# Kernel tuning notes

Measured on AMD Instinct MI355X. Metric: run time of the kernel, lower is better.

The kernel has to match this reference:

```python
import jax, jax.numpy as jnp
import numpy as np

N_NODES = 100000
N_EDGES = 3200000
D_FEAT = 128
N_CLASSES = 40


def setup_inputs() -> dict:
    key = jax.random.key(0)
    k1, k2, k3, k4 = jax.random.split(key, 4)
    x = jax.random.normal(k1, (N_NODES, D_FEAT), dtype=jnp.float32)
    edge_index = jax.random.randint(k2, (2, N_EDGES), 0, N_NODES, dtype=jnp.int64)
    # torch.nn.Linear default init ~ U(-1/sqrt(fan_in), 1/sqrt(fan_in)); randn is fine for a numeric baseline
    W = jax.random.normal(k3, (N_CLASSES, D_FEAT), dtype=jnp.float32) * (1.0 / np.sqrt(D_FEAT))
    b = jax.random.normal(k4, (N_CLASSES,), dtype=jnp.float32) * 0.01
    return {"x": x, "edge_index": edge_index, "W": W, "b": b, "K": 2}


def _sgc_forward(x, edge_index, W, b, K):
    N = x.shape[0]
    loop = jnp.arange(N, dtype=edge_index.dtype)
    # Outer add_self_loops in SGC.forward, then gcn_norm inside SGConv adds
    # self-loops AGAIN (PyG default add_self_loops=True) -> two self-loops per node.
    row = jnp.concatenate([edge_index[0], loop, loop])
    col = jnp.concatenate([edge_index[1], loop, loop])
    # gcn_norm: deg over destination (col) with unit edge weights
    deg = jax.ops.segment_sum(jnp.ones_like(row, dtype=x.dtype), col, num_segments=N)
    dinv = jnp.where(deg > 0, deg ** -0.5, 0.0)
    norm = dinv[row] * dinv[col]  # [E+2N]
    for _ in range(K):
        # out[col] += norm * x[row]  (K-hop symmetric-normalized propagation)
        x = jax.ops.segment_sum(norm[:, None] * x[row], col, num_segments=N)
    logits = x @ W.T + b  # [N, C]
    return jax.nn.log_softmax(logits, axis=1)


def reference(x, edge_index, W, b, K):
    return _sgc_forward(x, edge_index, W, b, K)
```

## Files before the change

### kernel.cpp

```cpp
#include <hip/hip_runtime.h>
#include <hip/hip_bf16.h>
#include <math.h>

#define DF 128
#define NC 40
#define PC 20
#define RB 8
#define RSZ 256
#define CHUNK 4096
#define CAP 12288

typedef float f32x4 __attribute__((ext_vector_type(4)));

__device__ __forceinline__ float bf2f(unsigned short h) {
  unsigned int u = ((unsigned int)h) << 16;
  union { unsigned int u; float f; } c; c.u = u; return c.f;
}
__device__ __forceinline__ unsigned short f2bf(float x) {
  union { float f; unsigned int u; } c; c.f = x;
  unsigned int u = c.u;
  return (unsigned short)((u + 0x7fffu + ((u >> 16) & 1u)) >> 16);
}
__device__ __forceinline__ float blo(unsigned int u) {
  union { unsigned int u; float f; } c; c.u = u << 16; return c.f;
}
__device__ __forceinline__ float bhi(unsigned int u) {
  union { unsigned int u; float f; } c; c.u = u & 0xffff0000u; return c.f;
}

__global__ __launch_bounds__(512) void k_binB(
    const int* __restrict__ row, const int* __restrict__ col,
    int* __restrict__ cnt, unsigned int* __restrict__ slab, int E, int NB) {
  __shared__ int colS[CHUNK];
  __shared__ int hist[512];
  __shared__ int cursor[512];
  int t = threadIdx.x;
  if (t < NB) hist[t] = 0;
  int s = blockIdx.x * CHUNK, e = min(E, s + CHUNK), n = e - s;
  for (int i = t; i < n; i += 512) colS[i] = col[s + i];
  __syncthreads();
  for (int i = t; i < n; i += 512) atomicAdd(&hist[colS[i] >> RB], 1);
  __syncthreads();
  if (t < NB) cursor[t] = hist[t] ? atomicAdd(&cnt[t], hist[t]) : 0;
  __syncthreads();
  for (int i = t; i < n; i += 512) {
    int c = colS[i];
    int b = c >> RB;
    int p = atomicAdd(&cursor[b], 1);
    slab[(size_t)b * CAP + p] = ((unsigned int)row[s + i] << RB) | (unsigned int)(c & (RSZ - 1));
  }
}

__global__ __launch_bounds__(512) void k_bucket_scan(
    const int* __restrict__ cnt, int* __restrict__ base,
    int* __restrict__ off, int NB, int N, int E) {
  __shared__ int s[512];
  int t = threadIdx.x;
  int v = (t < NB) ? cnt[t] : 0;
  s[t] = v;
  __syncthreads();
  for (int o = 1; o < 512; o <<= 1) {
    int u = (t >= o) ? s[t - o] : 0;
    __syncthreads();
    s[t] += u;
    __syncthreads();
  }
  if (t < NB) base[t] = s[t] - v;
  if (t == 0) { base[NB] = E; off[N] = E; }
}

__global__ __launch_bounds__(512) void k_binC(
    const unsigned int* __restrict__ slab, const int* __restrict__ base,
    int* __restrict__ off, int* __restrict__ eidx, float* __restrict__ dinv, int N) {
  __shared__ int hist[RSZ];
  __shared__ int sc[RSZ];
  __shared__ int cur[RSZ];
  int b = blockIdx.x;
  int t = threadIdx.x;
  if (t < RSZ) hist[t] = 0;
  __syncthreads();
  int cb = base[b], ce = base[b + 1];
  int cnt_b = ce - cb;
  const unsigned int* src = slab + (size_t)b * CAP;
  for (int i = t; i < cnt_b; i += 512) atomicAdd(&hist[src[i] & (RSZ - 1)], 1);
  __syncthreads();
  int v = (t < RSZ) ? hist[t] : 0;
  if (t < RSZ) sc[t] = v;
  __syncthreads();
  for (int o = 1; o < RSZ; o <<= 1) {
    int u = (t < RSZ && t >= o) ? sc[t - o] : 0;
    __syncthreads();
    if (t < RSZ) sc[t] += u;
    __syncthreads();
  }
  if (t < RSZ) {
    int pos = cb + sc[t] - v;
    int node = (b << RB) + t;
    if (node < N) {
      off[node] = pos;
      dinv[node] = rsqrtf((float)v + 2.0f);
    }
    cur[t] = pos;
  }
  __syncthreads();
  for (int i = t; i < cnt_b; i += 512) {
    unsigned int en = src[i];
    int p = atomicAdd(&cur[en & (RSZ - 1)], 1);
    eidx[p] = (int)(en >> RB);
  }
}

__global__ __launch_bounds__(128) void k_xw_scale(
    const float* __restrict__ x, const float* __restrict__ W,
    const float* __restrict__ dinv, unsigned short* __restrict__ g0, int N) {
  __shared__ float4 Ws[NC * (DF / 4)];
  for (int i = threadIdx.x; i < NC * (DF / 4); i += blockDim.x)
    Ws[i] = ((const float4*)W)[i];
  __syncthreads();
  int node = blockIdx.x * blockDim.x + threadIdx.x;
  if (node >= N) return;
  float acc[NC];
#pragma unroll
  for (int c = 0; c < NC; ++c) acc[c] = 0.f;
  const float4* xr = (const float4*)(x + (size_t)node * DF);
#pragma unroll 1
  for (int ch = 0; ch < 8; ++ch) {
    float4 v0 = xr[ch * 4 + 0];
    float4 v1 = xr[ch * 4 + 1];
    float4 v2 = xr[ch * 4 + 2];
    float4 v3 = xr[ch * 4 + 3];
#pragma unroll
    for (int c = 0; c < NC; ++c) {
      float4 w0 = Ws[c * (DF / 4) + ch * 4 + 0];
      float4 w1 = Ws[c * (DF / 4) + ch * 4 + 1];
      float4 w2 = Ws[c * (DF / 4) + ch * 4 + 2];
      float4 w3 = Ws[c * (DF / 4) + ch * 4 + 3];
      acc[c] += (v0.x * w0.x + v0.y * w0.y + v0.z * w0.z + v0.w * w0.w) +
                (v1.x * w1.x + v1.y * w1.y + v1.z * w1.z + v1.w * w1.w) +
                (v2.x * w2.x + v2.y * w2.y + v2.z * w2.z + v2.w * w2.w) +
                (v3.x * w3.x + v3.y * w3.y + v3.z * w3.z + v3.w * w3.w);
    }
  }
  float di = dinv[node];
  unsigned int pk[NC / 2];
#pragma unroll
  for (int c2 = 0; c2 < NC / 2; ++c2) {
    unsigned int lo = f2bf(di * acc[c2 * 2 + 0]);
    unsigned int hi = f2bf(di * acc[c2 * 2 + 1]);
    pk[c2] = lo | (hi << 16);
  }
  uint2* p0 = (uint2*)g0 + (size_t)node * 5;
  uint2* p1 = (uint2*)g0 + (size_t)N * 5 + (size_t)node * 5;
#pragma unroll
  for (int q = 0; q < 5; ++q) {
    p0[q] = make_uint2(pk[2 * q], pk[2 * q + 1]);
    p1[q] = make_uint2(pk[10 + 2 * q], pk[10 + 2 * q + 1]);
  }
}

template<int FINAL>
__global__ __launch_bounds__(256) void k_hop(
    const int* __restrict__ off, const int* __restrict__ eidx,
    const float* __restrict__ dinv, const unsigned short* __restrict__ gin,
    unsigned short* __restrict__ gout, float* __restrict__ logits,
    const float* __restrict__ bias, int N, int NBH) {
  int bid = blockIdx.x;
  int slot8 = bid & 7;
  int half = slot8 >> 2;
  int nbi = ((bid >> 3) << 2) + (slot8 & 3);
  if (nbi >= NBH) return;
  int lane = threadIdx.x & 63;
  int nA = (nbi << 3) + ((threadIdx.x >> 6) << 1);
  if (nA >= N) return;
  bool hasB = (nA + 1) < N;
  int nBs = hasB ? nA + 1 : nA;
  int slot = lane / 5;
  unsigned j = (unsigned)(lane - slot * 5);
  bool act = slot < 12;
  const uint2* plane = (const uint2*)gin + (size_t)half * ((size_t)N * 5);
  int sA = __builtin_amdgcn_readfirstlane(off[nA]);
  int eA = __builtin_amdgcn_readfirstlane(off[nA + 1]);
  int sB = eA;
  int eB = eA;
  if (hasB) eB = __builtin_amdgcn_readfirstlane(off[nA + 2]);
  float diA = dinv[nA];
  float diB = dinv[nBs];
  float4 bb;
  if (FINAL) bb = ((const float4*)bias)[half * 5 + (int)j];
  float A0 = 0.f, A1 = 0.f, A2 = 0.f, A3 = 0.f, A4 = 0.f, A5 = 0.f, A6 = 0.f, A7 = 0.f;
  float B0 = 0.f, B1 = 0.f, B2 = 0.f, B3 = 0.f, B4 = 0.f, B5 = 0.f, B6 = 0.f, B7 = 0.f;
  unsigned selfA = (unsigned)nA * 5u + j;
  unsigned selfB = (unsigned)nBs * 5u + j;
  if (slot == 0) {
    uint2 vA = plane[selfA];
    uint2 vB = plane[selfB];
    A0 = 2.f * blo(vA.x); A1 = 2.f * bhi(vA.x); A2 = 2.f * blo(vA.y); A3 = 2.f * bhi(vA.y);
    B0 = 2.f * blo(vB.x); B1 = 2.f * bhi(vB.x); B2 = 2.f * blo(vB.y); B3 = 2.f * bhi(vB.y);
  }
  int lastA = (eA > sA) ? eA - 1 : 0;
  int lastB = (eB > sB) ? eB - 1 : 0;
  {
    int pa0 = sA + slot, pa1 = pa0 + 12, pa2 = pa0 + 24, pa3 = pa0 + 36;
    int pb0 = sB + slot, pb1 = pb0 + 12, pb2 = pb0 + 24, pb3 = pb0 + 36;
    int ra0 = __builtin_nontemporal_load(eidx + min(pa0, lastA));
    int ra1 = __builtin_nontemporal_load(eidx + min(pa1, lastA));
    int ra2 = __builtin_nontemporal_load(eidx + min(pa2, lastA));
    int ra3 = __builtin_nontemporal_load(eidx + min(pa3, lastA));
    int rb0 = __builtin_nontemporal_load(eidx + min(pb0, lastB));
    int rb1 = __builtin_nontemporal_load(eidx + min(pb1, lastB));
    int rb2 = __builtin_nontemporal_load(eidx + min(pb2, lastB));
    int rb3 = __builtin_nontemporal_load(eidx + min(pb3, lastB));
    uint2 va0 = plane[(unsigned)ra0 * 5u + j];
    uint2 va1 = plane[(unsigned)ra1 * 5u + j];
    uint2 va2 = plane[(unsigned)ra2 * 5u + j];
    uint2 va3 = plane[(unsigned)ra3 * 5u + j];
    uint2 vb0 = plane[(unsigned)rb0 * 5u + j];
    uint2 vb1 = plane[(unsigned)rb1 * 5u + j];
    uint2 vb2 = plane[(unsigned)rb2 * 5u + j];
    uint2 vb3 = plane[(unsigned)rb3 * 5u + j];
    float ma0 = (act && pa0 < eA) ? 1.f : 0.f;
    float ma1 = (act && pa1 < eA) ? 1.f : 0.f;
    float ma2 = (act && pa2 < eA) ? 1.f : 0.f;
    float ma3 = (act && pa3 < eA) ? 1.f : 0.f;
    float mb0 = (act && pb0 < eB) ? 1.f : 0.f;
    float mb1 = (act && pb1 < eB) ? 1.f : 0.f;
    float mb2 = (act && pb2 < eB) ? 1.f : 0.f;
    float mb3 = (act && pb3 < eB) ? 1.f : 0.f;
    A0 += ma0 * blo(va0.x); A1 += ma0 * bhi(va0.x); A2 += ma0 * blo(va0.y); A3 += ma0 * bhi(va0.y);
    A0 += ma1 * blo(va1.x); A1 += ma1 * bhi(va1.x); A2 += ma1 * blo(va1.y); A3 += ma1 * bhi(va1.y);
    A4 += ma2 * blo(va2.x); A5 += ma2 * bhi(va2.x); A6 += ma2 * blo(va2.y); A7 += ma2 * bhi(va2.y);
    A4 += ma3 * blo(va3.x); A5 += ma3 * bhi(va3.x); A6 += ma3 * blo(va3.y); A7 += ma3 * bhi(va3.y);
    B0 += mb0 * blo(vb0.x); B1 += mb0 * bhi(vb0.x); B2 += mb0 * blo(vb0.y); B3 += mb0 * bhi(vb0.y);
    B0 += mb1 * blo(vb1.x); B1 += mb1 * bhi(vb1.x); B2 += mb1 * blo(vb1.y); B3 += mb1 * bhi(vb1.y);
    B4 += mb2 * blo(vb2.x); B5 += mb2 * bhi(vb2.x); B6 += mb2 * blo(vb2.y); B7 += mb2 * bhi(vb2.y);
    B4 += mb3 * blo(vb3.x); B5 += mb3 * bhi(vb3.x); B6 += mb3 * blo(vb3.y); B7 += mb3 * bhi(vb3.y);
  }
  for (int i = sA + 48; i < eA; i += 12) {
    int p = i + slot;
    int r = __builtin_nontemporal_load(eidx + min(p, lastA));
    uint2 v = plane[(unsigned)r * 5u + j];
    float m = (act && p < eA) ? 1.f : 0.f;
    A0 += m * blo(v.x); A1 += m * bhi(v.x); A2 += m * blo(v.y); A3 += m * bhi(v.y);
  }
  for (int i = sB + 48; i < eB; i += 12) {
    int p = i + slot;
    int r = __builtin_nontemporal_load(eidx + min(p, lastB));
    uint2 v = plane[(unsigned)r * 5u + j];
    float m = (act && p < eB) ? 1.f : 0.f;
    B0 += m * blo(v.x); B1 += m * bhi(v.x); B2 += m * blo(v.y); B3 += m * bhi(v.y);
  }
  float a0 = A0 + A4, a1 = A1 + A5, a2 = A2 + A6, a3 = A3 + A7;
  float b0 = B0 + B4, b1 = B1 + B5, b2 = B2 + B6, b3 = B3 + B7;
  int l30 = (lane + 30) & 63, l15 = (lane + 15) & 63;
  a0 += __shfl(a0, l30, 64); b0 += __shfl(b0, l30, 64);
  a1 += __shfl(a1, l30, 64); b1 += __shfl(b1, l30, 64);
  a2 += __shfl(a2, l30, 64); b2 += __shfl(b2, l30, 64);
  a3 += __shfl(a3, l30, 64); b3 += __shfl(b3, l30, 64);
  a0 += __shfl(a0, l15, 64); b0 += __shfl(b0, l15, 64);
  a1 += __shfl(a1, l15, 64); b1 += __shfl(b1, l15, 64);
  a2 += __shfl(a2, l15, 64); b2 += __shfl(b2, l15, 64);
  a3 += __shfl(a3, l15, 64); b3 += __shfl(b3, l15, 64);
  int l5 = (lane + 5) & 63, l10 = (lane + 10) & 63;
  a0 = a0 + __shfl(a0, l5, 64) + __shfl(a0, l10, 64);
  b0 = b0 + __shfl(b0, l5, 64) + __shfl(b0, l10, 64);
  a1 = a1 + __shfl(a1, l5, 64) + __shfl(a1, l10, 64);
  b1 = b1 + __shfl(b1, l5, 64) + __shfl(b1, l10, 64);
  a2 = a2 + __shfl(a2, l5, 64) + __shfl(a2, l10, 64);
  b2 = b2 + __shfl(b2, l5, 64) + __shfl(b2, l10, 64);
  a3 = a3 + __shfl(a3, l5, 64) + __shfl(a3, l10, 64);
  b3 = b3 + __shfl(b3, l5, 64) + __shfl(b3, l10, 64);
  if (slot == 0) {
    if (FINAL) {
      f32x4 lgA = { diA * a0 + bb.x, diA * a1 + bb.y, diA * a2 + bb.z, diA * a3 + bb.w };
      f32x4* dA = (f32x4*)(logits + (size_t)nA * NC + half * PC + 4u * j);
      __builtin_nontemporal_store(lgA, dA);
      if (hasB) {
        f32x4 lgB = { diB * b0 + bb.x, diB * b1 + bb.y, diB * b2 + bb.z, diB * b3 + bb.w };
        f32x4* dB = (f32x4*)(logits + (size_t)nBs * NC + half * PC + 4u * j);
        __builtin_nontemporal_store(lgB, dB);
      }
    } else {
      float scA = diA * diA;
      unsigned loA = (unsigned)f2bf(scA * a0) | ((unsigned)f2bf(scA * a1) << 16);
      unsigned hiA = (unsigned)f2bf(scA * a2) | ((unsigned)f2bf(scA * a3) << 16);
      unsigned long long pkA = (unsigned long long)loA | ((unsigned long long)hiA << 32);
      unsigned long long* dA =
          (unsigned long long*)((uint2*)gout + (size_t)half * ((size_t)N * 5) + selfA);
      __builtin_nontemporal_store(pkA, dA);
      if (hasB) {
        float scB = diB * diB;
        unsigned loB = (unsigned)f2bf(scB * b0) | ((unsigned)f2bf(scB * b1) << 16);
        unsigned hiB = (unsigned)f2bf(scB * b2) | ((unsigned)f2bf(scB * b3) << 16);
        unsigned long long pkB = (unsigned long long)loB | ((unsigned long long)hiB << 32);
        unsigned long long* dB =
            (unsigned long long*)((uint2*)gout + (size_t)half * ((size_t)N * 5) + selfB);
        __builtin_nontemporal_store(pkB, dB);
      }
    }
  }
}

__global__ __launch_bounds__(256) void k_lsm(
    const float* __restrict__ logits, float* __restrict__ out, int N) {
  int wave = (int)((blockIdx.x * (size_t)blockDim.x + threadIdx.x) >> 6);
  int lane = threadIdx.x & 63;
  if (wave >= N) return;
  bool act = lane < NC;
  float v = act ? __builtin_nontemporal_load(logits + (size_t)wave * NC + lane) : -3.0e38f;
  float m = v;
#pragma unroll
  for (int o = 32; o > 0; o >>= 1) m = fmaxf(m, __shfl_xor(m, o, 64));
  float ex = act ? expf(v - m) : 0.f;
  float ssum = ex;
#pragma unroll
  for (int o = 32; o > 0; o >>= 1) ssum += __shfl_xor(ssum, o, 64);
  float lse = m + logf(ssum);
  if (act) __builtin_nontemporal_store(v - lse, out + (size_t)wave * NC + lane);
}

extern "C" void kernel_launch(void* const* d_in, const int* in_sizes, int n_in,
                              void* d_out, int out_size, void* d_ws, size_t ws_size,
                              hipStream_t stream) {
  const float* x = (const float*)d_in[0];
  const int* ei  = (const int*)d_in[1];
  const float* W = (const float*)d_in[2];
  const float* b = (const float*)d_in[3];
  float* out = (float*)d_out;

  const int N = in_sizes[0] / DF;
  const int E = in_sizes[1] / 2;
  const int NB = (N + RSZ - 1) >> RB;
  const int* row  = ei;
  const int* colv = ei + E;

  char* basep = (char*)d_ws;
  auto alloc = [&](size_t bytes) {
    char* p = basep;
    basep += (bytes + 511) & ~(size_t)511;
    return p;
  };
  int*   cnt    = (int*)  alloc(((size_t)NB) * 4);
  int*   bbase  = (int*)  alloc(((size_t)NB + 1) * 4);
  unsigned int* slab = (unsigned int*)alloc((size_t)NB * CAP * 4);
  int*   off    = (int*)  alloc(((size_t)N + 1) * 4);
  int*   eidx   = (int*)  alloc((size_t)E * 4);
  float* dinv   = (float*)alloc((size_t)N * 4);
  unsigned short* g0 = (unsigned short*)alloc((size_t)N * NC * 2);
  unsigned short* g1 = (unsigned short*)alloc((size_t)N * NC * 2);
  float* logits = (float*)slab;

  const int gBin = (E + CHUNK - 1) / CHUNK;

  hipMemsetAsync(cnt, 0, (size_t)NB * 4, stream);
  k_binB<<<gBin, 512, 0, stream>>>(row, colv, cnt, slab, E, NB);
  k_bucket_scan<<<1, 512, 0, stream>>>(cnt, bbase, off, NB, N, E);
  k_binC<<<NB, 512, 0, stream>>>(slab, bbase, off, eidx, dinv, N);

  k_xw_scale<<<(N + 127) / 128, 128, 0, stream>>>(x, W, dinv, g0, N);

  const int NBH = (N + 7) >> 3;
  const int NBH4 = (NBH + 3) & ~3;
  const int gHop = 2 * NBH4;
  k_hop<0><<<gHop, 256, 0, stream>>>(off, eidx, dinv, g0, g1, nullptr, nullptr, N, NBH);
  k_hop<1><<<gHop, 256, 0, stream>>>(off, eidx, dinv, g1, nullptr, logits, b, N, NBH);

  const int gLsm = (int)(((size_t)N * 64 + 255) / 256);
  k_lsm<<<gLsm, 256, 0, stream>>>(logits, out, N);
}
```

Measured before the change: 370.9 us.

## Fold bucket scan into binC, prescale edge indices, two nodes per thread in xw

Drops the separate single-block bucket-scan kernel: each binC block now reduces the preceding bucket counts itself to get its base offset. Edge indices are stored premultiplied by the row byte stride, so the hop gather saves a multiply per edge. k_xw_scale now computes two nodes per thread to reuse each shared-memory W load. k_hop folds its accumulators from eight to four per node, and the self-loop load becomes unconditional with a multiplier mask. These remove a launch, some address arithmetic and LDS traffic, at the cost of more registers in xw and redundant prefix sums across blocks.

```diff
diff --git a/kernel.cpp b/kernel.cpp
--- a/kernel.cpp
+++ b/kernel.cpp
@@ -5,6 +5,7 @@
 #define DF 128
 #define NC 40
 #define PC 20
+#define PROWB 40
 #define RB 8
 #define RSZ 256
 #define CHUNK 4096
@@ -51,36 +52,26 @@
   }
 }
 
-__global__ __launch_bounds__(512) void k_bucket_scan(
-    const int* __restrict__ cnt, int* __restrict__ base,
-    int* __restrict__ off, int NB, int N, int E) {
-  __shared__ int s[512];
-  int t = threadIdx.x;
-  int v = (t < NB) ? cnt[t] : 0;
-  s[t] = v;
-  __syncthreads();
-  for (int o = 1; o < 512; o <<= 1) {
-    int u = (t >= o) ? s[t - o] : 0;
-    __syncthreads();
-    s[t] += u;
-    __syncthreads();
-  }
-  if (t < NB) base[t] = s[t] - v;
-  if (t == 0) { base[NB] = E; off[N] = E; }
-}
-
 __global__ __launch_bounds__(512) void k_binC(
-    const unsigned int* __restrict__ slab, const int* __restrict__ base,
-    int* __restrict__ off, int* __restrict__ eidx, float* __restrict__ dinv, int N) {
+    const unsigned int* __restrict__ slab, const int* __restrict__ cnt,
+    int* __restrict__ off, int* __restrict__ eidx, float* __restrict__ dinv,
+    int N, int NB, int E) {
+  __shared__ int redS[512];
   __shared__ int hist[RSZ];
   __shared__ int sc[RSZ];
   __shared__ int cur[RSZ];
   int b = blockIdx.x;
   int t = threadIdx.x;
+  redS[t] = (t < NB && t < b) ? cnt[t] : 0;
   if (t < RSZ) hist[t] = 0;
   __syncthreads();
-  int cb = base[b], ce = base[b + 1];
-  int cnt_b = ce - cb;
+  for (int o = 256; o > 0; o >>= 1) {
+    if (t < o) redS[t] += redS[t + o];
+    __syncthreads();
+  }
+  int cb = redS[0];
+  int cnt_b = cnt[b];
+  if (b == 0 && t == 0) off[N] = E;
   const unsigned int* src = slab + (size_t)b * CAP;
   for (int i = t; i < cnt_b; i += 512) atomicAdd(&hist[src[i] & (RSZ - 1)], 1);
   __syncthreads();
@@ -106,55 +97,81 @@
   for (int i = t; i < cnt_b; i += 512) {
     unsigned int en = src[i];
     int p = atomicAdd(&cur[en & (RSZ - 1)], 1);
-    eidx[p] = (int)(en >> RB);
+    eidx[p] = (int)((en >> RB) * (unsigned)PROWB);
   }
 }
 
 __global__ __launch_bounds__(128) void k_xw_scale(
     const float* __restrict__ x, const float* __restrict__ W,
-    const float* __restrict__ dinv, unsigned short* __restrict__ g0, int N) {
+    const float* __restrict__ dinv, unsigned short* __restrict__ g0,
+    int N, int NH) {
   __shared__ float4 Ws[NC * (DF / 4)];
   for (int i = threadIdx.x; i < NC * (DF / 4); i += blockDim.x)
     Ws[i] = ((const float4*)W)[i];
   __syncthreads();
-  int node = blockIdx.x * blockDim.x + threadIdx.x;
-  if (node >= N) return;
-  float acc[NC];
-#pragma unroll
-  for (int c = 0; c < NC; ++c) acc[c] = 0.f;
-  const float4* xr = (const float4*)(x + (size_t)node * DF);
+  int t = blockIdx.x * blockDim.x + threadIdx.x;
+  if (t >= NH) return;
+  int n0 = t;
+  int n1 = t + NH;
+  bool has1 = n1 < N;
+  int n1c = has1 ? n1 : n0;
+  float acc0[NC], acc1[NC];
+#pragma unroll
+  for (int c = 0; c < NC; ++c) { acc0[c] = 0.f; acc1[c] = 0.f; }
+  const float4* xr0 = (const float4*)(x + (size_t)n0 * DF);
+  const float4* xr1 = (const float4*)(x + (size_t)n1c * DF);
 #pragma unroll 1
   for (int ch = 0; ch < 8; ++ch) {
-    float4 v0 = xr[ch * 4 + 0];
-    float4 v1 = xr[ch * 4 + 1];
-    float4 v2 = xr[ch * 4 + 2];
-    float4 v3 = xr[ch * 4 + 3];
+    float4 a0 = xr0[ch * 4 + 0], a1 = xr0[ch * 4 + 1];
+    float4 a2 = xr0[ch * 4 + 2], a3 = xr0[ch * 4 + 3];
+    float4 b0 = xr1[ch * 4 + 0], b1 = xr1[ch * 4 + 1];
+    float4 b2 = xr1[ch * 4 + 2], b3 = xr1[ch * 4 + 3];
 #pragma unroll
     for (int c = 0; c < NC; ++c) {
       float4 w0 = Ws[c * (DF / 4) + ch * 4 + 0];
       float4 w1 = Ws[c * (DF / 4) + ch * 4 + 1];
       float4 w2 = Ws[c * (DF / 4) + ch * 4 + 2];
       float4 w3 = Ws[c * (DF / 4) + ch * 4 + 3];
-      acc[c] += (v0.x * w0.x + v0.y * w0.y + v0.z * w0.z + v0.w * w0.w) +
-                (v1.x * w1.x + v1.y * w1.y + v1.z * w1.z + v1.w * w1.w) +
-                (v2.x * w2.x + v2.y * w2.y + v2.z * w2.z + v2.w * w2.w) +
-                (v3.x * w3.x + v3.y * w3.y + v3.z * w3.z + v3.w * w3.w);
-    }
-  }
-  float di = dinv[node];
+      acc0[c] += (a0.x * w0.x + a0.y * w0.y + a0.z * w0.z + a0.w * w0.w) +
+                 (a1.x * w1.x + a1.y * w1.y + a1.z * w1.z + a1.w * w1.w) +
+                 (a2.x * w2.x + a2.y * w2.y + a2.z * w2.z + a2.w * w2.w) +
+                 (a3.x * w3.x + a3.y * w3.y + a3.z * w3.z + a3.w * w3.w);
+      acc1[c] += (b0.x * w0.x + b0.y * w0.y + b0.z * w0.z + b0.w * w0.w) +
+                 (b1.x * w1.x + b1.y * w1.y + b1.z * w1.z + b1.w * w1.w) +
+                 (b2.x * w2.x + b2.y * w2.y + b2.z * w2.z + b2.w * w2.w) +
+                 (b3.x * w3.x + b3.y * w3.y + b3.z * w3.z + b3.w * w3.w);
+    }
+  }
   unsigned int pk[NC / 2];
+  float di0 = dinv[n0];
 #pragma unroll
   for (int c2 = 0; c2 < NC / 2; ++c2) {
-    unsigned int lo = f2bf(di * acc[c2 * 2 + 0]);
-    unsigned int hi = f2bf(di * acc[c2 * 2 + 1]);
+    unsigned int lo = f2bf(di0 * acc0[c2 * 2 + 0]);
+    unsigned int hi = f2bf(di0 * acc0[c2 * 2 + 1]);
     pk[c2] = lo | (hi << 16);
   }
-  uint2* p0 = (uint2*)g0 + (size_t)node * 5;
-  uint2* p1 = (uint2*)g0 + (size_t)N * 5 + (size_t)node * 5;
+  uint2* q0 = (uint2*)g0 + (size_t)n0 * 5;
+  uint2* q1 = (uint2*)g0 + (size_t)N * 5 + (size_t)n0 * 5;
 #pragma unroll
   for (int q = 0; q < 5; ++q) {
-    p0[q] = make_uint2(pk[2 * q], pk[2 * q + 1]);
-    p1[q] = make_uint2(pk[10 + 2 * q], pk[10 + 2 * q + 1]);
+    q0[q] = make_uint2(pk[2 * q], pk[2 * q + 1]);
+    q1[q] = make_uint2(pk[10 + 2 * q], pk[10 + 2 * q + 1]);
+  }
+  if (has1) {
+    float di1 = dinv[n1];
+#pragma unroll
+    for (int c2 = 0; c2 < NC / 2; ++c2) {
+      unsigned int lo = f2bf(di1 * acc1[c2 * 2 + 0]);
+      unsigned int hi = f2bf(di1 * acc1[c2 * 2 + 1]);
+      pk[c2] = lo | (hi << 16);
+    }
+    uint2* r0 = (uint2*)g0 + (size_t)n1 * 5;
+    uint2* r1 = (uint2*)g0 + (size_t)N * 5 + (size_t)n1 * 5;
+#pragma unroll
+    for (int q = 0; q < 5; ++q) {
+      r0[q] = make_uint2(pk[2 * q], pk[2 * q + 1]);
+      r1[q] = make_uint2(pk[10 + 2 * q], pk[10 + 2 * q + 1]);
+    }
   }
 }
 
@@ -170,33 +187,28 @@
   int nbi = ((bid >> 3) << 2) + (slot8 & 3);
   if (nbi >= NBH) return;
   int lane = threadIdx.x & 63;
-  int nA = (nbi << 3) + ((threadIdx.x >> 6) << 1);
+  int nA = nbi * 8 + ((threadIdx.x >> 6) << 1);
   if (nA >= N) return;
   bool hasB = (nA + 1) < N;
-  int nBs = hasB ? nA + 1 : nA;
+  int nB = hasB ? nA + 1 : nA;
   int slot = lane / 5;
-  unsigned j = (unsigned)(lane - slot * 5);
+  int j = lane - slot * 5;
+  int j8 = j * 8;
   bool act = slot < 12;
-  const uint2* plane = (const uint2*)gin + (size_t)half * ((size_t)N * 5);
+  const char* plane = (const char*)gin + (size_t)half * ((size_t)N * PROWB);
   int sA = __builtin_amdgcn_readfirstlane(off[nA]);
   int eA = __builtin_amdgcn_readfirstlane(off[nA + 1]);
   int sB = eA;
-  int eB = eA;
-  if (hasB) eB = __builtin_amdgcn_readfirstlane(off[nA + 2]);
+  int eB = hasB ? __builtin_amdgcn_readfirstlane(off[nA + 2]) : eA;
   float diA = dinv[nA];
-  float diB = dinv[nBs];
-  float4 bb;
-  if (FINAL) bb = ((const float4*)bias)[half * 5 + (int)j];
-  float A0 = 0.f, A1 = 0.f, A2 = 0.f, A3 = 0.f, A4 = 0.f, A5 = 0.f, A6 = 0.f, A7 = 0.f;
-  float B0 = 0.f, B1 = 0.f, B2 = 0.f, B3 = 0.f, B4 = 0.f, B5 = 0.f, B6 = 0.f, B7 = 0.f;
-  unsigned selfA = (unsigned)nA * 5u + j;
-  unsigned selfB = (unsigned)nBs * 5u + j;
-  if (slot == 0) {
-    uint2 vA = plane[selfA];
-    uint2 vB = plane[selfB];
-    A0 = 2.f * blo(vA.x); A1 = 2.f * bhi(vA.x); A2 = 2.f * blo(vA.y); A3 = 2.f * bhi(vA.y);
-    B0 = 2.f * blo(vB.x); B1 = 2.f * bhi(vB.x); B2 = 2.f * blo(vB.y); B3 = 2.f * bhi(vB.y);
-  }
+  float diB = dinv[nB];
+  float mself = (slot == 0) ? 2.f : 0.f;
+  uint2 svA = *(const uint2*)(plane + (size_t)nA * PROWB + j8);
+  uint2 svB = *(const uint2*)(plane + (size_t)nB * PROWB + j8);
+  float A0 = mself * blo(svA.x), A1 = mself * bhi(svA.x);
+  float A2 = mself * blo(svA.y), A3 = mself * bhi(svA.y);
+  float B0 = mself * blo(svB.x), B1 = mself * bhi(svB.x);
+  float B2 = mself * blo(svB.y), B3 = mself * bhi(svB.y);
   int lastA = (eA > sA) ? eA - 1 : 0;
   int lastB = (eB > sB) ? eB - 1 : 0;
   {
@@ -210,14 +222,14 @@
     int rb1 = __builtin_nontemporal_load(eidx + min(pb1, lastB));
     int rb2 = __builtin_nontemporal_load(eidx + min(pb2, lastB));
     int rb3 = __builtin_nontemporal_load(eidx + min(pb3, lastB));
-    uint2 va0 = plane[(unsigned)ra0 * 5u + j];
-    uint2 va1 = plane[(unsigned)ra1 * 5u + j];
-    uint2 va2 = plane[(unsigned)ra2 * 5u + j];
-    uint2 va3 = plane[(unsigned)ra3 * 5u + j];
-    uint2 vb0 = plane[(unsigned)rb0 * 5u + j];
-    uint2 vb1 = plane[(unsigned)rb1 * 5u + j];
-    uint2 vb2 = plane[(unsigned)rb2 * 5u + j];
-    uint2 vb3 = plane[(unsigned)rb3 * 5u + j];
+    uint2 va0 = *(const uint2*)(plane + (unsigned)(ra0 + j8));
+    uint2 va1 = *(const uint2*)(plane + (unsigned)(ra1 + j8));
+    uint2 va2 = *(const uint2*)(plane + (unsigned)(ra2 + j8));
+    uint2 va3 = *(const uint2*)(plane + (unsigned)(ra3 + j8));
+    uint2 vb0 = *(const uint2*)(plane + (unsigned)(rb0 + j8));
+    uint2 vb1 = *(const uint2*)(plane + (unsigned)(rb1 + j8));
+    uint2 vb2 = *(const uint2*)(plane + (unsigned)(rb2 + j8));
+    uint2 vb3 = *(const uint2*)(plane + (unsigned)(rb3 + j8));
     float ma0 = (act && pa0 < eA) ? 1.f : 0.f;
     float ma1 = (act && pa1 < eA) ? 1.f : 0.f;
     float ma2 = (act && pa2 < eA) ? 1.f : 0.f;
@@ -228,73 +240,72 @@
     float mb3 = (act && pb3 < eB) ? 1.f : 0.f;
     A0 += ma0 * blo(va0.x); A1 += ma0 * bhi(va0.x); A2 += ma0 * blo(va0.y); A3 += ma0 * bhi(va0.y);
     A0 += ma1 * blo(va1.x); A1 += ma1 * bhi(va1.x); A2 += ma1 * blo(va1.y); A3 += ma1 * bhi(va1.y);
-    A4 += ma2 * blo(va2.x); A5 += ma2 * bhi(va2.x); A6 += ma2 * blo(va2.y); A7 += ma2 * bhi(va2.y);
-    A4 += ma3 * blo(va3.x); A5 += ma3 * bhi(va3.x); A6 += ma3 * blo(va3.y); A7 += ma3 * bhi(va3.y);
+    A0 += ma2 * blo(va2.x); A1 += ma2 * bhi(va2.x); A2 += ma2 * blo(va2.y); A3 += ma2 * bhi(va2.y);
+    A0 += ma3 * blo(va3.x); A1 += ma3 * bhi(va3.x); A2 += ma3 * blo(va3.y); A3 += ma3 * bhi(va3.y);
     B0 += mb0 * blo(vb0.x); B1 += mb0 * bhi(vb0.x); B2 += mb0 * blo(vb0.y); B3 += mb0 * bhi(vb0.y);
     B0 += mb1 * blo(vb1.x); B1 += mb1 * bhi(vb1.x); B2 += mb1 * blo(vb1.y); B3 += mb1 * bhi(vb1.y);
-    B4 += mb2 * blo(vb2.x); B5 += mb2 * bhi(vb2.x); B6 += mb2 * blo(vb2.y); B7 += mb2 * bhi(vb2.y);
-    B4 += mb3 * blo(vb3.x); B5 += mb3 * bhi(vb3.x); B6 += mb3 * blo(vb3.y); B7 += mb3 * bhi(vb3.y);
+    B0 += mb2 * blo(vb2.x); B1 += mb2 * bhi(vb2.x); B2 += mb2 * blo(vb2.y); B3 += mb2 * bhi(vb2.y);
+    B0 += mb3 * blo(vb3.x); B1 += mb3 * bhi(vb3.x); B2 += mb3 * blo(vb3.y); B3 += mb3 * bhi(vb3.y);
   }
   for (int i = sA + 48; i < eA; i += 12) {
     int p = i + slot;
     int r = __builtin_nontemporal_load(eidx + min(p, lastA));
-    uint2 v = plane[(unsigned)r * 5u + j];
+    uint2 v = *(const uint2*)(plane + (unsigned)(r + j8));
     float m = (act && p < eA) ? 1.f : 0.f;
     A0 += m * blo(v.x); A1 += m * bhi(v.x); A2 += m * blo(v.y); A3 += m * bhi(v.y);
   }
   for (int i = sB + 48; i < eB; i += 12) {
     int p = i + slot;
     int r = __builtin_nontemporal_load(eidx + min(p, lastB));
-    uint2 v = plane[(unsigned)r * 5u + j];
+    uint2 v = *(const uint2*)(plane + (unsigned)(r + j8));
     float m = (act && p < eB) ? 1.f : 0.f;
     B0 += m * blo(v.x); B1 += m * bhi(v.x); B2 += m * blo(v.y); B3 += m * bhi(v.y);
   }
-  float a0 = A0 + A4, a1 = A1 + A5, a2 = A2 + A6, a3 = A3 + A7;
-  float b0 = B0 + B4, b1 = B1 + B5, b2 = B2 + B6, b3 = B3 + B7;
   int l30 = (lane + 30) & 63, l15 = (lane + 15) & 63;
-  a0 += __shfl(a0, l30, 64); b0 += __shfl(b0, l30, 64);
-  a1 += __shfl(a1, l30, 64); b1 += __shfl(b1, l30, 64);
-  a2 += __shfl(a2, l30, 64); b2 += __shfl(b2, l30, 64);
-  a3 += __shfl(a3, l30, 64); b3 += __shfl(b3, l30, 64);
-  a0 += __shfl(a0, l15, 64); b0 += __shfl(b0, l15, 64);
-  a1 += __shfl(a1, l15, 64); b1 += __shfl(b1, l15, 64);
-  a2 += __shfl(a2, l15, 64); b2 += __shfl(b2, l15, 64);
-  a3 += __shfl(a3, l15, 64); b3 += __shfl(b3, l15, 64);
   int l5 = (lane + 5) & 63, l10 = (lane + 10) & 63;
-  a0 = a0 + __shfl(a0, l5, 64) + __shfl(a0, l10, 64);
-  b0 = b0 + __shfl(b0, l5, 64) + __shfl(b0, l10, 64);
-  a1 = a1 + __shfl(a1, l5, 64) + __shfl(a1, l10, 64);
-  b1 = b1 + __shfl(b1, l5, 64) + __shfl(b1, l10, 64);
-  a2 = a2 + __shfl(a2, l5, 64) + __shfl(a2, l10, 64);
-  b2 = b2 + __shfl(b2, l5, 64) + __shfl(b2, l10, 64);
-  a3 = a3 + __shfl(a3, l5, 64) + __shfl(a3, l10, 64);
-  b3 = b3 + __shfl(b3, l5, 64) + __shfl(b3, l10, 64);
+  A0 += __shfl(A0, l30, 64); B0 += __shfl(B0, l30, 64);
+  A1 += __shfl(A1, l30, 64); B1 += __shfl(B1, l30, 64);
+  A2 += __shfl(A2, l30, 64); B2 += __shfl(B2, l30, 64);
+  A3 += __shfl(A3, l30, 64); B3 += __shfl(B3, l30, 64);
+  A0 += __shfl(A0, l15, 64); B0 += __shfl(B0, l15, 64);
+  A1 += __shfl(A1, l15, 64); B1 += __shfl(B1, l15, 64);
+  A2 += __shfl(A2, l15, 64); B2 += __shfl(B2, l15, 64);
+  A3 += __shfl(A3, l15, 64); B3 += __shfl(B3, l15, 64);
+  A0 = A0 + __shfl(A0, l5, 64) + __shfl(A0, l10, 64);
+  B0 = B0 + __shfl(B0, l5, 64) + __shfl(B0, l10, 64);
+  A1 = A1 + __shfl(A1, l5, 64) + __shfl(A1, l10, 64);
+  B1 = B1 + __shfl(B1, l5, 64) + __shfl(B1, l10, 64);
+  A2 = A2 + __shfl(A2, l5, 64) + __shfl(A2, l10, 64);
+  B2 = B2 + __shfl(B2, l5, 64) + __shfl(B2, l10, 64);
+  A3 = A3 + __shfl(A3, l5, 64) + __shfl(A3, l10, 64);
+  B3 = B3 + __shfl(B3, l5, 64) + __shfl(B3, l10, 64);
   if (slot == 0) {
     if (FINAL) {
-      f32x4 lgA = { diA * a0 + bb.x, diA * a1 + bb.y, diA * a2 + bb.z, diA * a3 + bb.w };
-      f32x4* dA = (f32x4*)(logits + (size_t)nA * NC + half * PC + 4u * j);
-      __builtin_nontemporal_store(lgA, dA);
+      float4 bb = *(const float4*)(bias + half * PC + 4 * j);
+      f32x4 lgA = { diA * A0 + bb.x, diA * A1 + bb.y, diA * A2 + bb.z, diA * A3 + bb.w };
+      __builtin_nontemporal_store(lgA,
+          (f32x4*)(logits + (size_t)nA * NC + half * PC + 4 * j));
       if (hasB) {
-        f32x4 lgB = { diB * b0 + bb.x, diB * b1 + bb.y, diB * b2 + bb.z, diB * b3 + bb.w };
-        f32x4* dB = (f32x4*)(logits + (size_t)nBs * NC + half * PC + 4u * j);
-        __builtin_nontemporal_store(lgB, dB);
+        f32x4 lgB = { diB * B0 + bb.x, diB * B1 + bb.y, diB * B2 + bb.z, diB * B3 + bb.w };
+        __builtin_nontemporal_store(lgB,
+            (f32x4*)(logits + (size_t)nB * NC + half * PC + 4 * j));
       }
     } else {
       float scA = diA * diA;
-      unsigned loA = (unsigned)f2bf(scA * a0) | ((unsigned)f2bf(scA * a1) << 16);
-      unsigned hiA = (unsigned)f2bf(scA * a2) | ((unsigned)f2bf(scA * a3) << 16);
-      unsigned long long pkA = (unsigned long long)loA | ((unsigned long long)hiA << 32);
-      unsigned long long* dA =
-          (unsigned long long*)((uint2*)gout + (size_t)half * ((size_t)N * 5) + selfA);
-      __builtin_nontemporal_store(pkA, dA);
+      unsigned lo = (unsigned)f2bf(scA * A0) | ((unsigned)f2bf(scA * A1) << 16);
+      unsigned hi = (unsigned)f2bf(scA * A2) | ((unsigned)f2bf(scA * A3) << 16);
+      unsigned long long pk = (unsigned long long)lo | ((unsigned long long)hi << 32);
+      __builtin_nontemporal_store(pk,
+          (unsigned long long*)((char*)gout + (size_t)half * ((size_t)N * PROWB) +
+                                (size_t)nA * PROWB + j8));
       if (hasB) {
         float scB = diB * diB;
-        unsigned loB = (unsigned)f2bf(scB * b0) | ((unsigned)f2bf(scB * b1) << 16);
-        unsigned hiB = (unsigned)f2bf(scB * b2) | ((unsigned)f2bf(scB * b3) << 16);
-        unsigned long long pkB = (unsigned long long)loB | ((unsigned long long)hiB << 32);
-        unsigned long long* dB =
-            (unsigned long long*)((uint2*)gout + (size_t)half * ((size_t)N * 5) + selfB);
-        __builtin_nontemporal_store(pkB, dB);
+        unsigned lo2 = (unsigned)f2bf(scB * B0) | ((unsigned)f2bf(scB * B1) << 16);
+        unsigned hi2 = (unsigned)f2bf(scB * B2) | ((unsigned)f2bf(scB * B3) << 16);
+        unsigned long long pk2 = (unsigned long long)lo2 | ((unsigned long long)hi2 << 32);
+        __builtin_nontemporal_store(pk2,
+            (unsigned long long*)((char*)gout + (size_t)half * ((size_t)N * PROWB) +
+                                  (size_t)nB * PROWB + j8));
       }
     }
   }
@@ -340,7 +351,6 @@
     return p;
   };
   int*   cnt    = (int*)  alloc(((size_t)NB) * 4);
-  int*   bbase  = (int*)  alloc(((size_t)NB + 1) * 4);
   unsigned int* slab = (unsigned int*)alloc((size_t)NB * CAP * 4);
   int*   off    = (int*)  alloc(((size_t)N + 1) * 4);
   int*   eidx   = (int*)  alloc((size_t)E * 4);
@@ -353,10 +363,10 @@
 
   hipMemsetAsync(cnt, 0, (size_t)NB * 4, stream);
   k_binB<<<gBin, 512, 0, stream>>>(row, colv, cnt, slab, E, NB);
-  k_bucket_scan<<<1, 512, 0, stream>>>(cnt, bbase, off, NB, N, E);
-  k_binC<<<NB, 512, 0, stream>>>(slab, bbase, off, eidx, dinv, N);
-
-  k_xw_scale<<<(N + 127) / 128, 128, 0, stream>>>(x, W, dinv, g0, N);
+  k_binC<<<NB, 512, 0, stream>>>(slab, cnt, off, eidx, dinv, N, NB, E);
+
+  const int NH = (N + 1) / 2;
+  k_xw_scale<<<(NH + 127) / 128, 128, 0, stream>>>(x, W, dinv, g0, N, NH);
 
   const int NBH = (N + 7) >> 3;
   const int NBH4 = (NBH + 3) & ~3;
```

After: 362.3 us. -2.3%, faster.
